# Kernel tuning notes

Hardware: AMD Instinct MI355X
Metric: run time of the kernel (lower is better)

The kernel has to match this reference:

```python
import jax, jax.numpy as jnp
import numpy as np

DEPTH = 7  # leaves = 2**(DEPTH-1) = 64

def setup_inputs() -> dict:
    key = jax.random.key(0)
    k1, k2, k3 = jax.random.split(key, 3)
    bs, dimx, dimy = 32768, 2048, 2048
    leaves = 2 ** (DEPTH - 1)
    x = jax.random.normal(k1, (bs, dimx), dtype=jnp.float32)
    w = 0.1 * jax.random.uniform(k2, (dimx, leaves - 1), dtype=jnp.float32)
    b = jnp.zeros((leaves - 1,), dtype=jnp.float32)
    responses = 0.1 * jax.random.uniform(k3, (leaves, dimy), dtype=jnp.float32)
    return {"x": x, "w": w, "b": b, "responses": responses}

def reference(x, w, b, responses):
    bs = x.shape[0]
    # gate probabilities for all internal nodes of the binary tree: [bs, leaves-1]
    gate = jax.nn.sigmoid(x @ w + b)
    running = jnp.ones((bs, 1), dtype=x.dtype)
    for i in range(1, DEPTH):
        parents = gate[:, 2 ** (i - 1) - 1: 2 ** i - 1]  # [bs, 2**(i-1)]
        # torch.stack([left, right], dim=1).reshape -> [left | right] concat order
        running = jnp.concatenate([parents * running, (1.0 - parents) * running], axis=1)
    return running @ responses  # [bs, dimy]
```

## Files before the change

kernel.cpp:

```cpp
#include <hip/hip_runtime.h>
#include <hip/hip_bf16.h>


typedef short bf16x8 __attribute__((ext_vector_type(8)));
typedef float f32x4  __attribute__((ext_vector_type(4)));

#define BS    32768
#define DIMX  2048
#define NODES 63
#define NL    64
#define DIMY  2048

__device__ __forceinline__ unsigned short f2bf(float f) {
    union { float f; unsigned int u; } v; v.f = f;
    unsigned int r = v.u + 0x7FFFu + ((v.u >> 16) & 1u);
    return (unsigned short)(r >> 16);
}
__device__ __forceinline__ float bf2f(unsigned short h) {
    union { float f; unsigned int u; } v; v.u = ((unsigned int)h) << 16;
    return v.f;
}

__global__ __launch_bounds__(256) void prep(const float* __restrict__ w,
                                            const float* __restrict__ R,
                                            unsigned short* __restrict__ wTh,
                                            unsigned short* __restrict__ wTl,
                                            unsigned short* __restrict__ RTs) {
    int bid = blockIdx.x;
    int f = (bid & 511) * 256 + threadIdx.x;
    if (bid < 512) {
        int n = f >> 11;
        int k = f & 2047;
        float v = (n < NODES) ? w[(size_t)k * NODES + n] : 0.0f;
        unsigned short h = f2bf(v);
        wTh[f] = h;
        wTl[f] = f2bf(v - bf2f(h));
    } else {
        int e  = f & 7;
        int l  = (f >> 3) & 63;
        int kh = (f >> 9) & 1;
        int nf = f >> 10;
        int k  = kh * 32 + (l >> 4) * 8 + e;
        int n  = nf * 16 + (l & 15);
        RTs[f] = f2bf(R[(size_t)k * DIMY + n]);
    }
}

#define GBM   32
#define GBK   64
#define GLD   72
#define NSTEP (DIMX / GBK)

__device__ __forceinline__ bf16x8 pack8(float4 a, float4 b) {
    union { __hip_bfloat162 h2[4]; bf16x8 v; } u;
    u.h2[0] = __float22bfloat162_rn(make_float2(a.x, a.y));
    u.h2[1] = __float22bfloat162_rn(make_float2(a.z, a.w));
    u.h2[2] = __float22bfloat162_rn(make_float2(b.x, b.y));
    u.h2[3] = __float22bfloat162_rn(make_float2(b.z, b.w));
    return u.v;
}

__global__ __launch_bounds__(256, 4) void fused_kernel(const float* __restrict__ x,
                                                       const unsigned short* __restrict__ wTh,
                                                       const unsigned short* __restrict__ wTl,
                                                       const float* __restrict__ bias,
                                                       const unsigned short* __restrict__ RTs,
                                                       float* __restrict__ out) {
    __shared__ __align__(16) unsigned short xs[GBM][GLD];
    __shared__ __align__(16) unsigned short wsh[NL][GLD];
    __shared__ __align__(16) unsigned short wsl[NL][GLD];
    __shared__ float gl[GBM][NL + 1];

    const int t    = threadIdx.x;
    const int lane = t & 63;
    const int wv   = t >> 6;
    const int lr   = lane & 15;
    const int lg   = lane >> 4;
    const int m0   = blockIdx.x * GBM;
    const int rm   = wv & 1;
    const int cfp  = wv >> 1;

    const int xr = t >> 3;
    const int xc = (t & 7) * 8;
    const float* xsrc = x + (size_t)(m0 + xr) * DIMX + xc;
    const int wrA = t >> 3;
    const int wrB = wrA + 32;
    const int wc  = (t & 7) * 8;
    const unsigned short* hA = wTh + (size_t)wrA * DIMX + wc;
    const unsigned short* hB = wTh + (size_t)wrB * DIMX + wc;
    const unsigned short* lA = wTl + (size_t)wrA * DIMX + wc;
    const unsigned short* lB = wTl + (size_t)wrB * DIMX + wc;

    float4 rx0 = *(const float4*)(xsrc);
    float4 rx1 = *(const float4*)(xsrc + 4);
    uint4  rhA = *(const uint4*)(hA);
    uint4  rhB = *(const uint4*)(hB);
    uint4  rlA = *(const uint4*)(lA);
    uint4  rlB = *(const uint4*)(lB);

    f32x4 acc[2];
    acc[0] = (f32x4){0.f, 0.f, 0.f, 0.f};
    acc[1] = (f32x4){0.f, 0.f, 0.f, 0.f};

    for (int k = 0; k < NSTEP; ++k) {
        __syncthreads();
        *(bf16x8*)&xs[xr][xc]  = pack8(rx0, rx1);
        *(uint4*)&wsh[wrA][wc] = rhA;
        *(uint4*)&wsh[wrB][wc] = rhB;
        *(uint4*)&wsl[wrA][wc] = rlA;
        *(uint4*)&wsl[wrB][wc] = rlB;
        __syncthreads();
        if (k + 1 < NSTEP) {
            const int ko = (k + 1) * GBK;
            rx0 = *(const float4*)(xsrc + ko);
            rx1 = *(const float4*)(xsrc + ko + 4);
            rhA = *(const uint4*)(hA + ko);
            rhB = *(const uint4*)(hB + ko);
            rlA = *(const uint4*)(lA + ko);
            rlB = *(const uint4*)(lB + ko);
        }
        #pragma unroll
        for (int kk = 0; kk < GBK; kk += 32) {
            bf16x8 a = *(const bf16x8*)&xs[rm * 16 + lr][kk + lg * 8];
            #pragma unroll
            for (int ci = 0; ci < 2; ++ci) {
                const int brow = (cfp * 2 + ci) * 16 + lr;
                bf16x8 bh = *(const bf16x8*)&wsh[brow][kk + lg * 8];
                bf16x8 bo = *(const bf16x8*)&wsl[brow][kk + lg * 8];
                acc[ci] = __builtin_amdgcn_mfma_f32_16x16x32_bf16(a, bh, acc[ci], 0, 0, 0);
                acc[ci] = __builtin_amdgcn_mfma_f32_16x16x32_bf16(a, bo, acc[ci], 0, 0, 0);
            }
        }
    }

    #pragma unroll
    for (int ci = 0; ci < 2; ++ci) {
        const int col = cfp * 32 + ci * 16 + lr;
        const float bb = bias[col < NODES ? col : 0];
        #pragma unroll
        for (int i = 0; i < 4; ++i) {
            int row = rm * 16 + lg * 4 + i;
            float s = acc[ci][i] + bb;
            gl[row][col] = 1.0f / (1.0f + __expf(-s));
        }
    }
    __syncthreads();

    {
        const int rr  = t >> 3;
        const int sub = t & 7;
        const int b5 = sub & 1, b4 = (sub >> 1) & 1, mh = sub >> 2;
        const float* g = gl[rr];
        float a2[2], a4[4], a8[8];
        float g0 = g[0];
        a2[0] = g0; a2[1] = 1.f - g0;
        #pragma unroll
        for (int m = 0; m < 4; ++m) {
            float gg = g[1 + (m & 1)];
            a4[m] = a2[m & 1] * ((m & 2) ? (1.f - gg) : gg);
        }
        #pragma unroll
        for (int m = 0; m < 8; ++m) {
            float gg = g[3 + (m & 3)];
            a8[m] = a4[m & 3] * ((m & 4) ? (1.f - gg) : gg);
        }
        unsigned short o[8];
        #pragma unroll
        for (int j = 0; j < 8; ++j) {
            int m = mh * 8 + j;
            float g4 = g[7 + j];
            float p  = a8[j] * (mh ? (1.f - g4) : g4);
            float g5 = g[15 + m];
            p *= b4 ? (1.f - g5) : g5;
            float g6 = g[31 + m + 16 * b4];
            p *= b5 ? (1.f - g6) : g6;
            o[j] = f2bf(p);
        }
        uint4 q;
        q.x = (unsigned)o[0] | ((unsigned)o[1] << 16);
        q.y = (unsigned)o[2] | ((unsigned)o[3] << 16);
        q.z = (unsigned)o[4] | ((unsigned)o[5] << 16);
        q.w = (unsigned)o[6] | ((unsigned)o[7] << 16);
        *(uint4*)&xs[rr][b5 * 32 + b4 * 16 + mh * 8] = q;
    }
    __syncthreads();

    bf16x8 pa[2][2];
    #pragma unroll
    for (int rf = 0; rf < 2; ++rf)
        #pragma unroll
        for (int kh = 0; kh < 2; ++kh)
            pa[rf][kh] = *(const bf16x8*)&xs[rf * 16 + lr][kh * 32 + lg * 8];

    const unsigned short* bbase = RTs + (size_t)(wv * 4) * 512 + (size_t)lane * 8;
    #define BLD(s, ci, kh) (*(const bf16x8*)(bbase + (size_t)(((s) * 16 + (ci) * 2 + (kh))) * 512))

    bf16x8 cur[4], nxt[4];
    cur[0] = BLD(0, 0, 0); cur[1] = BLD(0, 0, 1);
    cur[2] = BLD(0, 1, 0); cur[3] = BLD(0, 1, 1);

    float* op = out + (size_t)(m0 + lg * 4) * DIMY + wv * 32 + lr;

    #pragma unroll
    for (int s = 0; s < 16; ++s) {
        if (s + 1 < 16) {
            nxt[0] = BLD(s + 1, 0, 0); nxt[1] = BLD(s + 1, 0, 1);
            nxt[2] = BLD(s + 1, 1, 0); nxt[3] = BLD(s + 1, 1, 1);
        }
        f32x4 oa[2][2];
        #pragma unroll
        for (int rf = 0; rf < 2; ++rf)
            #pragma unroll
            for (int ci = 0; ci < 2; ++ci) {
                oa[rf][ci] = (f32x4){0.f, 0.f, 0.f, 0.f};
                oa[rf][ci] = __builtin_amdgcn_mfma_f32_16x16x32_bf16(pa[rf][0], cur[ci * 2 + 0],
                                                                     oa[rf][ci], 0, 0, 0);
                oa[rf][ci] = __builtin_amdgcn_mfma_f32_16x16x32_bf16(pa[rf][1], cur[ci * 2 + 1],
                                                                     oa[rf][ci], 0, 0, 0);
            }
        #pragma unroll
        for (int rf = 0; rf < 2; ++rf)
            #pragma unroll
            for (int ci = 0; ci < 2; ++ci)
                #pragma unroll
                for (int i = 0; i < 4; ++i)
                    op[(size_t)(rf * 16 + i) * DIMY + s * 128 + ci * 16] = oa[rf][ci][i];
        #pragma unroll
        for (int q = 0; q < 4; ++q) cur[q] = nxt[q];
    }
    #undef BLD
}

extern "C" void kernel_launch(void* const* d_in, const int* in_sizes, int n_in,
                              void* d_out, int out_size, void* d_ws, size_t ws_size,
                              hipStream_t stream) {
    const float* x = (const float*)d_in[0];
    const float* w = (const float*)d_in[1];
    const float* b = (const float*)d_in[2];
    const float* R = (const float*)d_in[3];
    float* out = (float*)d_out;

    char* ws = (char*)d_ws;
    unsigned short* wTh = (unsigned short*)ws;
    unsigned short* wTl = (unsigned short*)(ws + 262144);
    unsigned short* RTs = (unsigned short*)(ws + 524288);

    prep<<<dim3(1024), 256, 0, stream>>>(w, R, wTh, wTl, RTs);
    fused_kernel<<<dim3(BS / GBM), 256, 0, stream>>>(x, wTh, wTl, b, RTs, out);
}
```

Baseline: 154.1 us.

## Preswizzle gate weights into MFMA fragment order and load directly from global

The prep kernel now writes the hi/lo bf16 split of the gate weights in MFMA B-fragment order, interleaved into a single buffer. The fused kernel reads the weight fragments straight from global/L2 into registers rather than staging them through shared memory, which removes two LDS tiles and their stores. With the smaller LDS footprint the occupancy hint is raised from 4 to 6 blocks. The cost is that each wave now issues per-iteration global loads with no prefetching, so latency may be exposed within the MFMA loop.

```diff
diff --git a/kernel.cpp b/kernel.cpp
--- a/kernel.cpp
+++ b/kernel.cpp
@@ -23,26 +23,30 @@
 
 __global__ __launch_bounds__(256) void prep(const float* __restrict__ w,
                                             const float* __restrict__ R,
-                                            unsigned short* __restrict__ wTh,
-                                            unsigned short* __restrict__ wTl,
+                                            unsigned short* __restrict__ wFs,
                                             unsigned short* __restrict__ RTs) {
-    int bid = blockIdx.x;
-    int f = (bid & 511) * 256 + threadIdx.x;
-    if (bid < 512) {
-        int n = f >> 11;
-        int k = f & 2047;
-        float v = (n < NODES) ? w[(size_t)k * NODES + n] : 0.0f;
+    int f = blockIdx.x * 256 + threadIdx.x;
+    if (f < 262144) {
+        int e   = f & 7;
+        int l   = (f >> 3) & 63;
+        int hl  = (f >> 9) & 1;
+        int g16 = (f >> 10) & 3;
+        int kk  = (f >> 12) & 1;
+        int k   = f >> 13;
+        int n    = g16 * 16 + (l & 15);
+        int kcol = k * 64 + kk * 32 + (l >> 4) * 8 + e;
+        float v = (n < NODES) ? w[(size_t)kcol * NODES + n] : 0.0f;
         unsigned short h = f2bf(v);
-        wTh[f] = h;
-        wTl[f] = f2bf(v - bf2f(h));
+        wFs[f] = hl ? f2bf(v - bf2f(h)) : h;
     } else {
-        int e  = f & 7;
-        int l  = (f >> 3) & 63;
-        int kh = (f >> 9) & 1;
-        int nf = f >> 10;
+        int f2 = f - 262144;
+        int e  = f2 & 7;
+        int l  = (f2 >> 3) & 63;
+        int kh = (f2 >> 9) & 1;
+        int nf = f2 >> 10;
         int k  = kh * 32 + (l >> 4) * 8 + e;
         int n  = nf * 16 + (l & 15);
-        RTs[f] = f2bf(R[(size_t)k * DIMY + n]);
+        RTs[f2] = f2bf(R[(size_t)k * DIMY + n]);
     }
 }
 
@@ -60,15 +64,12 @@
     return u.v;
 }
 
-__global__ __launch_bounds__(256, 4) void fused_kernel(const float* __restrict__ x,
-                                                       const unsigned short* __restrict__ wTh,
-                                                       const unsigned short* __restrict__ wTl,
+__global__ __launch_bounds__(256, 6) void fused_kernel(const float* __restrict__ x,
+                                                       const unsigned short* __restrict__ wFs,
                                                        const float* __restrict__ bias,
                                                        const unsigned short* __restrict__ RTs,
                                                        float* __restrict__ out) {
     __shared__ __align__(16) unsigned short xs[GBM][GLD];
-    __shared__ __align__(16) unsigned short wsh[NL][GLD];
-    __shared__ __align__(16) unsigned short wsl[NL][GLD];
     __shared__ float gl[GBM][NL + 1];
 
     const int t    = threadIdx.x;
@@ -83,20 +84,13 @@
     const int xr = t >> 3;
     const int xc = (t & 7) * 8;
     const float* xsrc = x + (size_t)(m0 + xr) * DIMX + xc;
-    const int wrA = t >> 3;
-    const int wrB = wrA + 32;
-    const int wc  = (t & 7) * 8;
-    const unsigned short* hA = wTh + (size_t)wrA * DIMX + wc;
-    const unsigned short* hB = wTh + (size_t)wrB * DIMX + wc;
-    const unsigned short* lA = wTl + (size_t)wrA * DIMX + wc;
-    const unsigned short* lB = wTl + (size_t)wrB * DIMX + wc;
+
+    const unsigned short* wb = wFs + (size_t)lane * 8;
+    #define WFRAG(k, kk, ci, hl) \
+        (*(const bf16x8*)(wb + (size_t)((((k) * 2 + (kk)) * 4 + (cfp * 2 + (ci))) * 2 + (hl)) * 512))
 
     float4 rx0 = *(const float4*)(xsrc);
     float4 rx1 = *(const float4*)(xsrc + 4);
-    uint4  rhA = *(const uint4*)(hA);
-    uint4  rhB = *(const uint4*)(hB);
-    uint4  rlA = *(const uint4*)(lA);
-    uint4  rlB = *(const uint4*)(lB);
 
     f32x4 acc[2];
     acc[0] = (f32x4){0.f, 0.f, 0.f, 0.f};
@@ -104,34 +98,26 @@
 
     for (int k = 0; k < NSTEP; ++k) {
         __syncthreads();
-        *(bf16x8*)&xs[xr][xc]  = pack8(rx0, rx1);
-        *(uint4*)&wsh[wrA][wc] = rhA;
-        *(uint4*)&wsh[wrB][wc] = rhB;
-        *(uint4*)&wsl[wrA][wc] = rlA;
-        *(uint4*)&wsl[wrB][wc] = rlB;
+        *(bf16x8*)&xs[xr][xc] = pack8(rx0, rx1);
         __syncthreads();
         if (k + 1 < NSTEP) {
             const int ko = (k + 1) * GBK;
             rx0 = *(const float4*)(xsrc + ko);
             rx1 = *(const float4*)(xsrc + ko + 4);
-            rhA = *(const uint4*)(hA + ko);
-            rhB = *(const uint4*)(hB + ko);
-            rlA = *(const uint4*)(lA + ko);
-            rlB = *(const uint4*)(lB + ko);
-        }
-        #pragma unroll
-        for (int kk = 0; kk < GBK; kk += 32) {
-            bf16x8 a = *(const bf16x8*)&xs[rm * 16 + lr][kk + lg * 8];
+        }
+        #pragma unroll
+        for (int kk = 0; kk < 2; ++kk) {
+            bf16x8 a = *(const bf16x8*)&xs[rm * 16 + lr][kk * 32 + lg * 8];
             #pragma unroll
             for (int ci = 0; ci < 2; ++ci) {
-                const int brow = (cfp * 2 + ci) * 16 + lr;
-                bf16x8 bh = *(const bf16x8*)&wsh[brow][kk + lg * 8];
-                bf16x8 bo = *(const bf16x8*)&wsl[brow][kk + lg * 8];
+                bf16x8 bh = WFRAG(k, kk, ci, 0);
+                bf16x8 bo = WFRAG(k, kk, ci, 1);
                 acc[ci] = __builtin_amdgcn_mfma_f32_16x16x32_bf16(a, bh, acc[ci], 0, 0, 0);
                 acc[ci] = __builtin_amdgcn_mfma_f32_16x16x32_bf16(a, bo, acc[ci], 0, 0, 0);
             }
         }
     }
+    #undef WFRAG
 
     #pragma unroll
     for (int ci = 0; ci < 2; ++ci) {
@@ -241,10 +227,9 @@
     float* out = (float*)d_out;
 
     char* ws = (char*)d_ws;
-    unsigned short* wTh = (unsigned short*)ws;
-    unsigned short* wTl = (unsigned short*)(ws + 262144);
+    unsigned short* wFs = (unsigned short*)ws;
     unsigned short* RTs = (unsigned short*)(ws + 524288);
 
-    prep<<<dim3(1024), 256, 0, stream>>>(w, R, wTh, wTl, RTs);
-    fused_kernel<<<dim3(BS / GBM), 256, 0, stream>>>(x, wTh, wTl, b, RTs, out);
-}
+    prep<<<dim3(1536), 256, 0, stream>>>(w, R, wFs, RTs);
+    fused_kernel<<<dim3(BS / GBM), 256, 0, stream>>>(x, wFs, b, RTs, out);
+}
```

New measurement: 155.7 us. About the same (+1.0%).
